# Kernel tuning notes

Hardware: AMD Instinct MI355X
Metric: run time of the kernel (lower is better)

Reference implementation:

```python
import jax, jax.numpy as jnp
import numpy as np

B, L, D = 1, 4096, 1024
H, HD = 16, 64

def setup_inputs() -> dict:
    key = jax.random.key(0)
    ks = jax.random.split(key, 5)
    scale = 1.0 / np.sqrt(D)
    return {
        "x": jax.random.normal(ks[0], (B, L, D), dtype=jnp.float32),
        "Wq": jax.random.normal(ks[1], (D, D), dtype=jnp.float32) * scale,
        "Wk": jax.random.normal(ks[2], (D, D), dtype=jnp.float32) * scale,
        "Wv": jax.random.normal(ks[3], (D, D), dtype=jnp.float32) * scale,
        "Wo": jax.random.normal(ks[4], (D, D), dtype=jnp.float32) * scale,
    }

def reference(x, Wq, Wk, Wv, Wo):
    Bc, Lc, _ = x.shape
    # torch Linear: y = x @ W.T
    q = (x @ Wq.T).reshape(Bc, Lc, H, HD).transpose(0, 2, 1, 3)  # [B,H,L,hd]
    k = (x @ Wk.T).reshape(Bc, Lc, H, HD).transpose(0, 2, 1, 3)
    v = (x @ Wv.T).reshape(Bc, Lc, H, HD).transpose(0, 2, 1, 3)
    scale = HD ** -0.5
    scores = jnp.einsum('bhqd,bhkd->bhqk', q, k) * scale  # [B,H,L,L]
    causal = jnp.tril(jnp.ones((Lc, Lc), dtype=bool))
    scores = jnp.where(causal, scores, -jnp.inf)
    attn = jax.nn.softmax(scores, axis=-1)
    out = jnp.einsum('bhqk,bhkd->bhqd', attn, v)
    out = out.transpose(0, 2, 1, 3).reshape(Bc, Lc, H * HD)
    return out @ Wo.T
```

## Files before the change

kernel.cpp:

```cpp
#include <hip/hip_runtime.h>
#include <hip/hip_bf16.h>
#include <stdint.h>

#define L_SEQ   4096
#define D_MODEL 1024
#define N_HEADS 16
#define HEAD_DIM 64

typedef uint16_t u16;
typedef __bf16 bf16x8 __attribute__((ext_vector_type(8)));
typedef short s16x4 __attribute__((ext_vector_type(4)));
typedef float floatx4 __attribute__((ext_vector_type(4)));

__device__ __forceinline__ floatx4 mfma32(bf16x8 a, bf16x8 b, floatx4 c) {
  return __builtin_amdgcn_mfma_f32_16x16x32_bf16(a, b, c, 0, 0, 0);
}

__device__ __forceinline__ floatx4 mfma16(s16x4 a, s16x4 b, floatx4 c) {
#if __has_builtin(__builtin_amdgcn_mfma_f32_16x16x16bf16_1k)
  return __builtin_amdgcn_mfma_f32_16x16x16bf16_1k(a, b, c, 0, 0, 0);
#else
  floatx4 d;
  asm volatile("v_mfma_f32_16x16x16_bf16 %0, %1, %2, %3"
               : "=v"(d) : "v"(a), "v"(b), "v"(c));
  return d;
#endif
}

__device__ __forceinline__ float hw_exp2(float x) {
  return __builtin_amdgcn_exp2f(x);
}

__device__ __forceinline__ uint32_t fbits(float f) {
  union { float f; uint32_t u; } x; x.f = f; return x.u;
}

__device__ __forceinline__ uint32_t pack_bf16_trunc(float f1, float f0) {
  return __builtin_amdgcn_perm(fbits(f1), fbits(f0), 0x07060302u);
}

__device__ __forceinline__ void load16_lds(const u16* g, u16* l) {
  __builtin_amdgcn_global_load_lds(
      (const __attribute__((address_space(1))) void*)g,
      (__attribute__((address_space(3))) void*)l, 16, 0, 0);
}

__device__ __forceinline__ u16 f2bf(float f) {
  uint32_t u = fbits(f);
  uint32_t r = u + 0x7FFFu + ((u >> 16) & 1u);
  return (u16)(r >> 16);
}

#define Q_PRESCALE 0.18033688011112042f
#define SM_SHIFT   8.0f

__global__ __launch_bounds__(256) void cvt_kernel(
    const float* __restrict__ x,  const float* __restrict__ wq,
    const float* __restrict__ wk, const float* __restrict__ wv,
    const float* __restrict__ wo,
    u16* __restrict__ xb, u16* __restrict__ wqb, u16* __restrict__ wkb,
    u16* __restrict__ wvb, u16* __restrict__ wob) {
  const int z = blockIdx.z;
  const float* s; u16* d; int n;
  if (z == 0)      { s = x;  d = xb;  n = L_SEQ * D_MODEL; }
  else if (z == 1) { s = wq; d = wqb; n = D_MODEL * D_MODEL; }
  else if (z == 2) { s = wk; d = wkb; n = D_MODEL * D_MODEL; }
  else if (z == 3) { s = wv; d = wvb; n = D_MODEL * D_MODEL; }
  else             { s = wo; d = wob; n = D_MODEL * D_MODEL; }
  const int stride = gridDim.x * 256 * 4;
  for (int i = (blockIdx.x * 256 + threadIdx.x) * 4; i < n; i += stride) {
    float4 v = *(const float4*)(s + i);
    ushort4 o;
    o.x = f2bf(v.x); o.y = f2bf(v.y); o.z = f2bf(v.z); o.w = f2bf(v.w);
    *(ushort4*)(d + i) = o;
  }
}

__global__ __launch_bounds__(256) void qkv_gemm_kernel(
    const u16* __restrict__ X,
    const u16* __restrict__ Wq, const u16* __restrict__ Wk, const u16* __restrict__ Wv,
    u16* __restrict__ Qo, u16* __restrict__ Ko, u16* __restrict__ VTo) {
  constexpr int BK = 32, Kdim = D_MODEL;
  __shared__ __align__(16) u16 As[128 * BK];
  __shared__ __align__(16) u16 Bs[128 * BK];

  const int z = blockIdx.z;
  const u16* __restrict__ A;
  const u16* __restrict__ B;
  int m0, n0;
  if (z < 2) { A = X; B = z ? Wk : Wq; m0 = blockIdx.x * 128; n0 = blockIdx.y * 128; }
  else       { A = Wv; B = X;          m0 = blockIdx.y * 128; n0 = blockIdx.x * 128; }

  const int tid = threadIdx.x;
  const int wave = tid >> 6, lane = tid & 63;
  const int wm = wave & 1, wn = wave >> 1;
  const int quad = lane >> 4, l15 = lane & 15;

  floatx4 acc[4][4] = {};

  const int cbase = wave * 128;
  const int c0 = cbase + lane, c1 = c0 + 64;
  const int r0 = c0 >> 2, cc0 = (c0 & 3) * 8;
  const int r1 = c1 >> 2, cc1 = (c1 & 3) * 8;

  for (int k0 = 0; k0 < Kdim; k0 += BK) {
    load16_lds(&A[(size_t)(m0 + r0) * Kdim + k0 + cc0], &As[cbase * 8]);
    load16_lds(&A[(size_t)(m0 + r1) * Kdim + k0 + cc1], &As[(cbase + 64) * 8]);
    load16_lds(&B[(size_t)(n0 + r0) * Kdim + k0 + cc0], &Bs[cbase * 8]);
    load16_lds(&B[(size_t)(n0 + r1) * Kdim + k0 + cc1], &Bs[(cbase + 64) * 8]);
    __syncthreads();

    bf16x8 af[4], wf[4];
#pragma unroll
    for (int i = 0; i < 4; ++i)
      af[i] = *(const bf16x8*)(&As[(wm * 64 + i * 16 + l15) * BK + quad * 8]);
#pragma unroll
    for (int j = 0; j < 4; ++j)
      wf[j] = *(const bf16x8*)(&Bs[(wn * 64 + j * 16 + l15) * BK + quad * 8]);
#pragma unroll
    for (int i = 0; i < 4; ++i)
#pragma unroll
      for (int j = 0; j < 4; ++j)
        acc[i][j] = mfma32(af[i], wf[j], acc[i][j]);
    __syncthreads();
  }

  const float scale = (z == 0) ? Q_PRESCALE : 1.0f;
  u16* __restrict__ C = (z == 0) ? Qo : (z == 1) ? Ko : VTo;
#pragma unroll
  for (int i = 0; i < 4; ++i) {
    const int mb = m0 + wm * 64 + i * 16 + quad * 4;
#pragma unroll
    for (int j = 0; j < 4; ++j) {
      const int n = n0 + wn * 64 + j * 16 + l15;
#pragma unroll
      for (int r = 0; r < 4; ++r) {
        const int m = mb + r;
        if (z < 2) {
          C[(size_t)(n >> 6) * (size_t)L_SEQ * HEAD_DIM + (size_t)m * HEAD_DIM + (n & 63)] =
              f2bf(acc[i][j][r] * scale);
        } else {
          C[(size_t)(m >> 6) * (size_t)L_SEQ * HEAD_DIM + (size_t)(m & 63) * L_SEQ + n] =
              f2bf(acc[i][j][r]);
        }
      }
    }
  }
}

__global__ __launch_bounds__(256) void out_gemm_kernel(
    const u16* __restrict__ A, const u16* __restrict__ W, float* __restrict__ C) {
  constexpr int BK = 32, Kdim = D_MODEL;
  __shared__ __align__(16) u16 As[128 * BK];
  __shared__ __align__(16) u16 Bs[64 * BK];

  const int tid = threadIdx.x;
  const int wave = tid >> 6, lane = tid & 63;
  const int wm = wave & 1, wn = wave >> 1;
  const int quad = lane >> 4, l15 = lane & 15;
  const int m0 = blockIdx.x * 128, n0 = blockIdx.y * 64;

  floatx4 acc[4][2] = {};

  const int cbase = wave * 128;
  const int c0 = cbase + lane, c1 = c0 + 64;
  const int ra0 = c0 >> 2, ca0 = (c0 & 3) * 8;
  const int ra1 = c1 >> 2, ca1 = (c1 & 3) * 8;
  const int cb = wave * 64 + lane;
  const int rb = cb >> 2, cbcol = (cb & 3) * 8;

  for (int k0 = 0; k0 < Kdim; k0 += BK) {
    load16_lds(&A[(size_t)(m0 + ra0) * Kdim + k0 + ca0], &As[cbase * 8]);
    load16_lds(&A[(size_t)(m0 + ra1) * Kdim + k0 + ca1], &As[(cbase + 64) * 8]);
    load16_lds(&W[(size_t)(n0 + rb) * Kdim + k0 + cbcol], &Bs[wave * 64 * 8]);
    __syncthreads();

    bf16x8 af[4], wf[2];
#pragma unroll
    for (int i = 0; i < 4; ++i)
      af[i] = *(const bf16x8*)(&As[(wm * 64 + i * 16 + l15) * BK + quad * 8]);
#pragma unroll
    for (int j = 0; j < 2; ++j)
      wf[j] = *(const bf16x8*)(&Bs[(wn * 32 + j * 16 + l15) * BK + quad * 8]);
#pragma unroll
    for (int i = 0; i < 4; ++i)
#pragma unroll
      for (int j = 0; j < 2; ++j)
        acc[i][j] = mfma32(af[i], wf[j], acc[i][j]);
    __syncthreads();
  }

#pragma unroll
  for (int i = 0; i < 4; ++i) {
    const int mb = m0 + wm * 64 + i * 16 + quad * 4;
#pragma unroll
    for (int j = 0; j < 2; ++j) {
      const int n = n0 + wn * 32 + j * 16 + l15;
#pragma unroll
      for (int r = 0; r < 4; ++r)
        C[(size_t)(mb + r) * D_MODEL + n] = acc[i][j][r];
    }
  }
}

#define LDP 72
__global__ __launch_bounds__(256) void attn_kernel(
    const u16* __restrict__ Q, const u16* __restrict__ K,
    const u16* __restrict__ VT, u16* __restrict__ Oa) {
  __shared__ __align__(16) u16 Ks[64 * LDP];
  __shared__ __align__(16) u16 Vts[64 * LDP];
  __shared__ __align__(16) float Of[4 * 2 * 64 * 16];
  __shared__ float Lf[4 * 64 + 64];

  const int h = blockIdx.y;
  const int bx = blockIdx.x;
  const int tid = threadIdx.x;
  const int wave = tid >> 6, lane = tid & 63;
  const int quad = lane >> 4, l15 = lane & 15;

  const size_t hoff = (size_t)h * L_SEQ * HEAD_DIM;
  const u16* __restrict__ Qh = Q + hoff;
  const u16* __restrict__ Kh = K + hoff;
  const u16* __restrict__ VTh = VT + hoff;

  const int kc0 = lane, kc1 = lane + 64;
  const int krow0 = wave * 16 + (kc0 >> 3), kcol0 = (kc0 & 7) * 8;
  const int krow1 = wave * 16 + (kc1 >> 3), kcol1 = (kc1 & 7) * 8;
  const int vd0 = lane >> 1, vk = (lane & 1) * 8;
  u16* const KsW0 = &Ks[krow0 * LDP + kcol0];
  u16* const KsW1 = &Ks[krow1 * LDP + kcol1];
  u16* const VsW0 = &Vts[vd0 * LDP + wave * 16 + vk];
  u16* const VsW1 = &Vts[(vd0 + 32) * LDP + wave * 16 + vk];
  const u16* const Kg0 = Kh + (size_t)krow0 * HEAD_DIM + kcol0;
  const u16* const Kg1 = Kh + (size_t)krow1 * HEAD_DIM + kcol1;
  const u16* const Vg0 = VTh + (size_t)vd0 * L_SEQ + wave * 16 + vk;
  const u16* const Vg1 = VTh + (size_t)(vd0 + 32) * L_SEQ + wave * 16 + vk;

  for (int half = 0; half < 2; ++half) {
    const int qt = half ? (63 - bx) : bx;
    const int q0 = qt * 64;

    bf16x8 qf[4][2];
#pragma unroll
    for (int jq = 0; jq < 4; ++jq) {
      const u16* qrow = Qh + (size_t)(q0 + jq * 16 + l15) * HEAD_DIM;
      qf[jq][0] = *(const bf16x8*)(qrow + quad * 8);
      qf[jq][1] = *(const bf16x8*)(qrow + 32 + quad * 8);
    }

    floatx4 oacc[4][4] = {};
    float psum[4] = {};

    float4 ka = *(const float4*)(Kg0);
    float4 kb = *(const float4*)(Kg1);
    float4 va = *(const float4*)(Vg0);
    float4 vb4 = *(const float4*)(Vg1);

    for (int kt = 0; kt <= qt; ++kt) {
      *(float4*)KsW0 = ka;
      *(float4*)KsW1 = kb;
      *(float4*)VsW0 = va;
      *(float4*)VsW1 = vb4;
      if (kt < qt) {
        const size_t ko = (size_t)(kt + 1) * 64;
        ka  = *(const float4*)(Kg0 + ko * HEAD_DIM);
        kb  = *(const float4*)(Kg1 + ko * HEAD_DIM);
        va  = *(const float4*)(Vg0 + ko);
        vb4 = *(const float4*)(Vg1 + ko);
      }

      bf16x8 kf0 = *(const bf16x8*)(&Ks[(wave * 16 + l15) * LDP + quad * 8]);
      bf16x8 kf1 = *(const bf16x8*)(&Ks[(wave * 16 + l15) * LDP + 32 + quad * 8]);

      floatx4 s[4];
#pragma unroll
      for (int jq = 0; jq < 4; ++jq) {
        floatx4 z = {};
        z = mfma32(kf0, qf[jq][0], z);
        z = mfma32(kf1, qf[jq][1], z);
        s[jq] = z;
      }

      if (kt == qt) {
        const int keyw = wave * 16 + quad * 4;
#pragma unroll
        for (int jq = 0; jq < 4; ++jq) {
          const int qloc = jq * 16 + l15;
#pragma unroll
          for (int r = 0; r < 4; ++r)
            if (keyw + r > qloc) s[jq][r] = -1e30f;
        }
      }

      s16x4 pa[4];
#pragma unroll
      for (int jq = 0; jq < 4; ++jq) {
        float p0 = hw_exp2(s[jq][0] - SM_SHIFT);
        float p1 = hw_exp2(s[jq][1] - SM_SHIFT);
        float p2 = hw_exp2(s[jq][2] - SM_SHIFT);
        float p3 = hw_exp2(s[jq][3] - SM_SHIFT);
        psum[jq] += (p0 + p1) + (p2 + p3);
        union { uint32_t w[2]; s16x4 v; } pu;
        pu.w[0] = pack_bf16_trunc(p1, p0);
        pu.w[1] = pack_bf16_trunc(p3, p2);
        pa[jq] = pu.v;
      }

      s16x4 vb[4];
#pragma unroll
      for (int nt = 0; nt < 4; ++nt)
        vb[nt] = *(const s16x4*)(&Vts[(nt * 16 + l15) * LDP + wave * 16 + quad * 4]);
#pragma unroll
      for (int jq = 0; jq < 4; ++jq)
#pragma unroll
        for (int nt = 0; nt < 4; ++nt)
          oacc[jq][nt] = mfma16(pa[jq], vb[nt], oacc[jq][nt]);
    }

#pragma unroll
    for (int jq = 0; jq < 4; ++jq) {
      psum[jq] += __shfl_xor(psum[jq], 16, 64);
      psum[jq] += __shfl_xor(psum[jq], 32, 64);
    }
    __syncthreads();
    if (quad == 0) {
#pragma unroll
      for (int jq = 0; jq < 4; ++jq)
        Lf[wave * 64 + jq * 16 + l15] = psum[jq];
    }
    __syncthreads();
    if (tid < 64) {
      float lt = Lf[tid] + Lf[64 + tid] + Lf[128 + tid] + Lf[192 + tid];
      Lf[256 + tid] = 1.0f / lt;
    }

    const int qc = tid >> 2, d4 = (tid & 3) * 4;
#pragma unroll
    for (int pass = 0; pass < 2; ++pass) {
#pragma unroll
      for (int sl = 0; sl < 2; ++sl) {
        const int nt = pass * 2 + sl;
#pragma unroll
        for (int jq = 0; jq < 4; ++jq)
#pragma unroll
          for (int r = 0; r < 4; ++r)
            Of[wave * 2048 + sl * 1024 + (jq * 16 + quad * 4 + r) * 16 + l15] =
                oacc[jq][nt][r];
      }
      __syncthreads();
      const float invq = Lf[256 + qc];
#pragma unroll
      for (int sl = 0; sl < 2; ++sl) {
        floatx4 a0 = *(const floatx4*)&Of[0 * 2048 + sl * 1024 + qc * 16 + d4];
        floatx4 a1 = *(const floatx4*)&Of[1 * 2048 + sl * 1024 + qc * 16 + d4];
        floatx4 a2 = *(const floatx4*)&Of[2 * 2048 + sl * 1024 + qc * 16 + d4];
        floatx4 a3 = *(const floatx4*)&Of[3 * 2048 + sl * 1024 + qc * 16 + d4];
        floatx4 sum = (a0 + a1) + (a2 + a3);
        ushort4 o;
        o.x = f2bf(sum[0] * invq); o.y = f2bf(sum[1] * invq);
        o.z = f2bf(sum[2] * invq); o.w = f2bf(sum[3] * invq);
        *(ushort4*)(Oa + (size_t)(q0 + qc) * D_MODEL + (size_t)h * HEAD_DIM +
                    (pass * 2 + sl) * 16 + d4) = o;
      }
      __syncthreads();
    }
  }
}

extern "C" void kernel_launch(void* const* d_in, const int* in_sizes, int n_in,
                              void* d_out, int out_size, void* d_ws, size_t ws_size,
                              hipStream_t stream) {
  const float* x  = (const float*)d_in[0];
  const float* Wq = (const float*)d_in[1];
  const float* Wk = (const float*)d_in[2];
  const float* Wv = (const float*)d_in[3];
  const float* Wo = (const float*)d_in[4];
  float* out = (float*)d_out;

  const size_t XN = (size_t)L_SEQ * D_MODEL;
  const size_t WN = (size_t)D_MODEL * D_MODEL;
  const size_t HLHD = (size_t)N_HEADS * L_SEQ * HEAD_DIM;

  u16* x_bf  = (u16*)d_ws;
  u16* wq_bf = x_bf + XN;
  u16* wk_bf = wq_bf + WN;
  u16* wv_bf = wk_bf + WN;
  u16* wo_bf = wv_bf + WN;
  u16* q_ws  = wo_bf + WN;
  u16* k_ws  = q_ws + HLHD;
  u16* vT_ws = k_ws + HLHD;
  u16* a_ws  = vT_ws + HLHD;

  dim3 gc(1024, 1, 5);
  cvt_kernel<<<gc, 256, 0, stream>>>(x, Wq, Wk, Wv, Wo,
                                     x_bf, wq_bf, wk_bf, wv_bf, wo_bf);

  dim3 gqkv(L_SEQ / 128, D_MODEL / 128, 3);
  qkv_gemm_kernel<<<gqkv, 256, 0, stream>>>(x_bf, wq_bf, wk_bf, wv_bf,
                                            q_ws, k_ws, vT_ws);

  dim3 ga(32, N_HEADS, 1);
  attn_kernel<<<ga, 256, 0, stream>>>(q_ws, k_ws, vT_ws, a_ws);

  dim3 go(L_SEQ / 128, D_MODEL / 64, 1);
  out_gemm_kernel<<<go, 256, 0, stream>>>(a_ws, wo_bf, out);
}
```

Before: 215.5 us.

## Restructure attention: one query tile per block, direct K loads, MFMA row sums

The attention kernel now gives each block a single query tile, launching twice as many blocks, with the longest tiles scheduled first instead of pairing a short and a long tile. K fragments are loaded straight from global memory into registers, which drops the K shared-memory staging. Softmax row sums are computed with an MFMA against a ones vector rather than scalar adds and shuffles, the fixed exponent shift is removed, and the output-reduction buffer is halved with one reduction pass per column tile. Launch bounds request 4 blocks per CU to raise occupancy; the risks are less balanced per-block work and possible exp overflow without the shift.

```diff
diff --git a/kernel.cpp b/kernel.cpp
--- a/kernel.cpp
+++ b/kernel.cpp
@@ -52,7 +52,6 @@
 }
 
 #define Q_PRESCALE 0.18033688011112042f
-#define SM_SHIFT   8.0f
 
 __global__ __launch_bounds__(256) void cvt_kernel(
     const float* __restrict__ x,  const float* __restrict__ wq,
@@ -204,16 +203,16 @@
 }
 
 #define LDP 72
-__global__ __launch_bounds__(256) void attn_kernel(
+__global__ __launch_bounds__(256, 4) void attn_kernel(
     const u16* __restrict__ Q, const u16* __restrict__ K,
     const u16* __restrict__ VT, u16* __restrict__ Oa) {
-  __shared__ __align__(16) u16 Ks[64 * LDP];
   __shared__ __align__(16) u16 Vts[64 * LDP];
-  __shared__ __align__(16) float Of[4 * 2 * 64 * 16];
+  __shared__ __align__(16) float Of[4 * 64 * 16];
   __shared__ float Lf[4 * 64 + 64];
 
   const int h = blockIdx.y;
-  const int bx = blockIdx.x;
+  const int qt = 63 - blockIdx.x;
+  const int q0 = qt * 64;
   const int tid = threadIdx.x;
   const int wave = tid >> 6, lane = tid & 63;
   const int quad = lane >> 4, l15 = lane & 15;
@@ -223,147 +222,122 @@
   const u16* __restrict__ Kh = K + hoff;
   const u16* __restrict__ VTh = VT + hoff;
 
-  const int kc0 = lane, kc1 = lane + 64;
-  const int krow0 = wave * 16 + (kc0 >> 3), kcol0 = (kc0 & 7) * 8;
-  const int krow1 = wave * 16 + (kc1 >> 3), kcol1 = (kc1 & 7) * 8;
+  bf16x8 qf[4][2];
+#pragma unroll
+  for (int jq = 0; jq < 4; ++jq) {
+    const u16* qrow = Qh + (size_t)(q0 + jq * 16 + l15) * HEAD_DIM;
+    qf[jq][0] = *(const bf16x8*)(qrow + quad * 8);
+    qf[jq][1] = *(const bf16x8*)(qrow + 32 + quad * 8);
+  }
+
+  const u16* const Kg = Kh + (size_t)(wave * 16 + l15) * HEAD_DIM;
   const int vd0 = lane >> 1, vk = (lane & 1) * 8;
-  u16* const KsW0 = &Ks[krow0 * LDP + kcol0];
-  u16* const KsW1 = &Ks[krow1 * LDP + kcol1];
   u16* const VsW0 = &Vts[vd0 * LDP + wave * 16 + vk];
   u16* const VsW1 = &Vts[(vd0 + 32) * LDP + wave * 16 + vk];
-  const u16* const Kg0 = Kh + (size_t)krow0 * HEAD_DIM + kcol0;
-  const u16* const Kg1 = Kh + (size_t)krow1 * HEAD_DIM + kcol1;
   const u16* const Vg0 = VTh + (size_t)vd0 * L_SEQ + wave * 16 + vk;
   const u16* const Vg1 = VTh + (size_t)(vd0 + 32) * L_SEQ + wave * 16 + vk;
 
-  for (int half = 0; half < 2; ++half) {
-    const int qt = half ? (63 - bx) : bx;
-    const int q0 = qt * 64;
-
-    bf16x8 qf[4][2];
+  floatx4 oacc[4][4] = {};
+  floatx4 lacc[4] = {};
+
+  const s16x4 ones = {(short)0x3F80, (short)0x3F80, (short)0x3F80, (short)0x3F80};
+
+  bf16x8 kc0 = *(const bf16x8*)(Kg + quad * 8);
+  bf16x8 kc1 = *(const bf16x8*)(Kg + 32 + quad * 8);
+  float4 va  = *(const float4*)(Vg0);
+  float4 vb4 = *(const float4*)(Vg1);
+
+  for (int kt = 0; kt <= qt; ++kt) {
+    *(float4*)VsW0 = va;
+    *(float4*)VsW1 = vb4;
+    bf16x8 kf0 = kc0, kf1 = kc1;
+    if (kt < qt) {
+      const u16* Kn = Kg + (size_t)(kt + 1) * 64 * HEAD_DIM;
+      kc0 = *(const bf16x8*)(Kn + quad * 8);
+      kc1 = *(const bf16x8*)(Kn + 32 + quad * 8);
+      va  = *(const float4*)(Vg0 + (size_t)(kt + 1) * 64);
+      vb4 = *(const float4*)(Vg1 + (size_t)(kt + 1) * 64);
+    }
+
+    floatx4 s[4];
 #pragma unroll
     for (int jq = 0; jq < 4; ++jq) {
-      const u16* qrow = Qh + (size_t)(q0 + jq * 16 + l15) * HEAD_DIM;
-      qf[jq][0] = *(const bf16x8*)(qrow + quad * 8);
-      qf[jq][1] = *(const bf16x8*)(qrow + 32 + quad * 8);
-    }
-
-    floatx4 oacc[4][4] = {};
-    float psum[4] = {};
-
-    float4 ka = *(const float4*)(Kg0);
-    float4 kb = *(const float4*)(Kg1);
-    float4 va = *(const float4*)(Vg0);
-    float4 vb4 = *(const float4*)(Vg1);
-
-    for (int kt = 0; kt <= qt; ++kt) {
-      *(float4*)KsW0 = ka;
-      *(float4*)KsW1 = kb;
-      *(float4*)VsW0 = va;
-      *(float4*)VsW1 = vb4;
-      if (kt < qt) {
-        const size_t ko = (size_t)(kt + 1) * 64;
-        ka  = *(const float4*)(Kg0 + ko * HEAD_DIM);
-        kb  = *(const float4*)(Kg1 + ko * HEAD_DIM);
-        va  = *(const float4*)(Vg0 + ko);
-        vb4 = *(const float4*)(Vg1 + ko);
+      floatx4 z = {};
+      z = mfma32(kf0, qf[jq][0], z);
+      z = mfma32(kf1, qf[jq][1], z);
+      s[jq] = z;
+    }
+
+    if (kt == qt) {
+      const int keyw = wave * 16 + quad * 4;
+#pragma unroll
+      for (int jq = 0; jq < 4; ++jq) {
+        const int qloc = jq * 16 + l15;
+#pragma unroll
+        for (int r = 0; r < 4; ++r)
+          if (keyw + r > qloc) s[jq][r] = -1e30f;
       }
-
-      bf16x8 kf0 = *(const bf16x8*)(&Ks[(wave * 16 + l15) * LDP + quad * 8]);
-      bf16x8 kf1 = *(const bf16x8*)(&Ks[(wave * 16 + l15) * LDP + 32 + quad * 8]);
-
-      floatx4 s[4];
-#pragma unroll
-      for (int jq = 0; jq < 4; ++jq) {
-        floatx4 z = {};
-        z = mfma32(kf0, qf[jq][0], z);
-        z = mfma32(kf1, qf[jq][1], z);
-        s[jq] = z;
-      }
-
-      if (kt == qt) {
-        const int keyw = wave * 16 + quad * 4;
-#pragma unroll
-        for (int jq = 0; jq < 4; ++jq) {
-          const int qloc = jq * 16 + l15;
-#pragma unroll
-          for (int r = 0; r < 4; ++r)
-            if (keyw + r > qloc) s[jq][r] = -1e30f;
-        }
-      }
-
-      s16x4 pa[4];
-#pragma unroll
-      for (int jq = 0; jq < 4; ++jq) {
-        float p0 = hw_exp2(s[jq][0] - SM_SHIFT);
-        float p1 = hw_exp2(s[jq][1] - SM_SHIFT);
-        float p2 = hw_exp2(s[jq][2] - SM_SHIFT);
-        float p3 = hw_exp2(s[jq][3] - SM_SHIFT);
-        psum[jq] += (p0 + p1) + (p2 + p3);
-        union { uint32_t w[2]; s16x4 v; } pu;
-        pu.w[0] = pack_bf16_trunc(p1, p0);
-        pu.w[1] = pack_bf16_trunc(p3, p2);
-        pa[jq] = pu.v;
-      }
-
-      s16x4 vb[4];
+    }
+
+    s16x4 pa[4];
+#pragma unroll
+    for (int jq = 0; jq < 4; ++jq) {
+      float p0 = hw_exp2(s[jq][0]);
+      float p1 = hw_exp2(s[jq][1]);
+      float p2 = hw_exp2(s[jq][2]);
+      float p3 = hw_exp2(s[jq][3]);
+      union { uint32_t w[2]; s16x4 v; } pu;
+      pu.w[0] = pack_bf16_trunc(p1, p0);
+      pu.w[1] = pack_bf16_trunc(p3, p2);
+      pa[jq] = pu.v;
+      lacc[jq] = mfma16(pa[jq], ones, lacc[jq]);
+    }
+
+    s16x4 vb[4];
+#pragma unroll
+    for (int nt = 0; nt < 4; ++nt)
+      vb[nt] = *(const s16x4*)(&Vts[(nt * 16 + l15) * LDP + wave * 16 + quad * 4]);
+#pragma unroll
+    for (int jq = 0; jq < 4; ++jq)
 #pragma unroll
       for (int nt = 0; nt < 4; ++nt)
-        vb[nt] = *(const s16x4*)(&Vts[(nt * 16 + l15) * LDP + wave * 16 + quad * 4]);
-#pragma unroll
-      for (int jq = 0; jq < 4; ++jq)
-#pragma unroll
-        for (int nt = 0; nt < 4; ++nt)
-          oacc[jq][nt] = mfma16(pa[jq], vb[nt], oacc[jq][nt]);
-    }
-
-#pragma unroll
-    for (int jq = 0; jq < 4; ++jq) {
-      psum[jq] += __shfl_xor(psum[jq], 16, 64);
-      psum[jq] += __shfl_xor(psum[jq], 32, 64);
-    }
-    __syncthreads();
-    if (quad == 0) {
-#pragma unroll
-      for (int jq = 0; jq < 4; ++jq)
-        Lf[wave * 64 + jq * 16 + l15] = psum[jq];
-    }
-    __syncthreads();
-    if (tid < 64) {
-      float lt = Lf[tid] + Lf[64 + tid] + Lf[128 + tid] + Lf[192 + tid];
-      Lf[256 + tid] = 1.0f / lt;
-    }
-
-    const int qc = tid >> 2, d4 = (tid & 3) * 4;
-#pragma unroll
-    for (int pass = 0; pass < 2; ++pass) {
-#pragma unroll
-      for (int sl = 0; sl < 2; ++sl) {
-        const int nt = pass * 2 + sl;
-#pragma unroll
-        for (int jq = 0; jq < 4; ++jq)
-#pragma unroll
-          for (int r = 0; r < 4; ++r)
-            Of[wave * 2048 + sl * 1024 + (jq * 16 + quad * 4 + r) * 16 + l15] =
-                oacc[jq][nt][r];
-      }
-      __syncthreads();
-      const float invq = Lf[256 + qc];
-#pragma unroll
-      for (int sl = 0; sl < 2; ++sl) {
-        floatx4 a0 = *(const floatx4*)&Of[0 * 2048 + sl * 1024 + qc * 16 + d4];
-        floatx4 a1 = *(const floatx4*)&Of[1 * 2048 + sl * 1024 + qc * 16 + d4];
-        floatx4 a2 = *(const floatx4*)&Of[2 * 2048 + sl * 1024 + qc * 16 + d4];
-        floatx4 a3 = *(const floatx4*)&Of[3 * 2048 + sl * 1024 + qc * 16 + d4];
-        floatx4 sum = (a0 + a1) + (a2 + a3);
-        ushort4 o;
-        o.x = f2bf(sum[0] * invq); o.y = f2bf(sum[1] * invq);
-        o.z = f2bf(sum[2] * invq); o.w = f2bf(sum[3] * invq);
-        *(ushort4*)(Oa + (size_t)(q0 + qc) * D_MODEL + (size_t)h * HEAD_DIM +
-                    (pass * 2 + sl) * 16 + d4) = o;
-      }
-      __syncthreads();
-    }
+        oacc[jq][nt] = mfma16(pa[jq], vb[nt], oacc[jq][nt]);
+  }
+
+  if (l15 == 0) {
+#pragma unroll
+    for (int jq = 0; jq < 4; ++jq)
+#pragma unroll
+      for (int r = 0; r < 4; ++r)
+        Lf[wave * 64 + jq * 16 + quad * 4 + r] = lacc[jq][r];
+  }
+  __syncthreads();
+  if (tid < 64) {
+    float lt = Lf[tid] + Lf[64 + tid] + Lf[128 + tid] + Lf[192 + tid];
+    Lf[256 + tid] = 1.0f / lt;
+  }
+
+  const int qc = tid >> 2, d4 = (tid & 3) * 4;
+#pragma unroll
+  for (int nt = 0; nt < 4; ++nt) {
+#pragma unroll
+    for (int jq = 0; jq < 4; ++jq)
+#pragma unroll
+      for (int r = 0; r < 4; ++r)
+        Of[wave * 1024 + (jq * 16 + quad * 4 + r) * 16 + l15] = oacc[jq][nt][r];
+    __syncthreads();
+    const float invq = Lf[256 + qc];
+    floatx4 a0 = *(const floatx4*)&Of[0 * 1024 + qc * 16 + d4];
+    floatx4 a1 = *(const floatx4*)&Of[1 * 1024 + qc * 16 + d4];
+    floatx4 a2 = *(const floatx4*)&Of[2 * 1024 + qc * 16 + d4];
+    floatx4 a3 = *(const floatx4*)&Of[3 * 1024 + qc * 16 + d4];
+    floatx4 sum = (a0 + a1) + (a2 + a3);
+    ushort4 o;
+    o.x = f2bf(sum[0] * invq); o.y = f2bf(sum[1] * invq);
+    o.z = f2bf(sum[2] * invq); o.w = f2bf(sum[3] * invq);
+    *(ushort4*)(Oa + (size_t)(q0 + qc) * D_MODEL + (size_t)h * HEAD_DIM +
+                nt * 16 + d4) = o;
+    __syncthreads();
   }
 }
 
@@ -399,7 +373,7 @@
   qkv_gemm_kernel<<<gqkv, 256, 0, stream>>>(x_bf, wq_bf, wk_bf, wv_bf,
                                             q_ws, k_ws, vT_ws);
 
-  dim3 ga(32, N_HEADS, 1);
+  dim3 ga(64, N_HEADS, 1);
   attn_kernel<<<ga, 256, 0, stream>>>(q_ws, k_ws, vT_ws, a_ws);
 
   dim3 go(L_SEQ / 128, D_MODEL / 64, 1);
```

Result: slower. 468.8 us (+117.5%).
